# Performance work log

Hardware: AMD Instinct MI355X
Metric: run time of the kernel (lower is better)

## Reference

```python
import jax, jax.numpy as jnp
import numpy as np

B = 1024
IN_Q = 2048
IN_KV = 2048
NH = 16
D = 64
INNER = NH * D
TF = 4
NC = 2
EPS = 1e-5
SLOPE = 0.01  # LeakyReLU default negative slope


def setup_inputs() -> dict:
    key = jax.random.key(0)
    ks = jax.random.split(key, 8)
    s = 0.02
    return {
        "q_input": jax.random.normal(ks[0], (B, IN_Q), jnp.float32),
        "kv_input": jax.random.normal(ks[1], (B, IN_KV), jnp.float32),
        "Wq": jax.random.normal(ks[2], (INNER, IN_Q), jnp.float32) * s,
        "bq": jax.random.normal(ks[3], (INNER,), jnp.float32) * s,
        "Wkv": jax.random.normal(ks[4], (2 * INNER, IN_KV), jnp.float32) * s,
        "bkv": jax.random.normal(ks[5], (2 * INNER,), jnp.float32) * s,
        "bn_w": jnp.ones((TF,), jnp.float32),
        "bn_b": jnp.zeros((TF,), jnp.float32),
        "Wo": jax.random.normal(ks[6], (NC, TF), jnp.float32) * s,
        "bo": jax.random.normal(ks[7], (NC,), jnp.float32) * s,
    }


def reference(q_input, kv_input, Wq, bq, Wkv, bkv, bn_w, bn_b, Wo, bo):
    b = q_input.shape[0]
    # projections: [B, NH, D] and [B, NH, 2D]
    q = (q_input @ Wq.T + bq).reshape(b, NH, D)
    kv = (kv_input @ Wkv.T + bkv).reshape(b, NH, 2 * D)
    k, v = kv[..., :D], kv[..., D:]
    # sim[b,n] = k[b,n,:] . q[b,n,:]  (per-head scalar score)
    sim = jnp.einsum("bnd,bnd->bn", k, q)
    att = jax.nn.softmax(sim, axis=-1)  # softmax over heads
    # torch.matmul([B,NH], [B,NH,D]) broadcast -> out[i,j,:] = sum_n att[j,n] v[i,n,:]
    att_out = jnp.einsum("jn,ind->ijd", att, v)  # [B, B, D]
    flat = att_out.reshape(b, b * D)  # [B, B*D]
    # AdaptiveAvgPool1d to TF bins (L % TF == 0 -> exact reshape-mean)
    pooled = flat.reshape(b, TF, (b * D) // TF).mean(axis=-1)  # [B, TF]
    x = jnp.where(pooled >= 0, pooled, SLOPE * pooled)  # LeakyReLU
    # BatchNorm1d, train mode (batch stats, biased variance)
    mean = x.mean(axis=0)
    var = x.var(axis=0)
    x = (x - mean) * jax.lax.rsqrt(var + EPS) * bn_w + bn_b
    # dropout(p=0.0) is identity
    return x @ Wo.T + bo  # [B, NC]
```

## Files before the change

kernel.cpp:

```cpp
#include <hip/hip_runtime.h>
#include <hip/hip_bf16.h>

#define EPS 1e-5f
#define SLOPE 0.01f

typedef __attribute__((ext_vector_type(8))) short bfrag8;
typedef __attribute__((ext_vector_type(4))) float f32x4;

#define WS_SIM_OFF   0u
#define WS_S_OFF     65536u
#define WS_WVS_OFF   131072u
#define WS_BVS_OFF   262144u
#define WS_AIMG_OFF  262208u
#define WS_BIMG_OFF  8650816u

__device__ __forceinline__ unsigned short f2bf(float f) {
    union { float f; unsigned int u; } x; x.f = f;
    unsigned int r = (x.u + 0x7FFFu + ((x.u >> 16) & 1u)) >> 16;
    return (unsigned short)r;
}
__device__ __forceinline__ uint4 pack8(const float4& a, const float4& b) {
    uint4 r;
    r.x = (unsigned)f2bf(a.x) | ((unsigned)f2bf(a.y) << 16);
    r.y = (unsigned)f2bf(a.z) | ((unsigned)f2bf(a.w) << 16);
    r.z = (unsigned)f2bf(b.x) | ((unsigned)f2bf(b.y) << 16);
    r.w = (unsigned)f2bf(b.z) | ((unsigned)f2bf(b.w) << 16);
    return r;
}

#define PREP_A   524288
#define PREP_B2  (PREP_A + 524288)
#define PREP_WVSE (PREP_B2 + 32768)
#define PREP_SIME (PREP_WVSE + 16384)
#define PREP_END  (PREP_SIME + 16)

__global__ __launch_bounds__(256) void prep_kernel(
        const float* __restrict__ qin, const float* __restrict__ kvin,
        const float* __restrict__ Wq, const float* __restrict__ Wkv,
        const float* __restrict__ bkv, unsigned char* __restrict__ ws) {
    int gid = blockIdx.x * 256 + threadIdx.x;
    if (gid < PREP_A) {
        int l  = gid & 63;
        int mi = (gid >> 6) & 1;
        int ks = (gid >> 7) & 1;
        int kt = (gid >> 8) & 31;
        int rm = (gid >> 13) & 1;
        int mbb = (gid >> 14) & 15;
        int qq = gid >> 18;
        int row = mbb * 64 + rm * 32 + mi * 16 + (l & 15);
        int k0  = kt * 64 + ks * 32 + (l >> 4) * 8;
        const float* src = (qq ? kvin : qin) + (size_t)row * 2048 + k0;
        float4 v0 = *(const float4*)src;
        float4 v1 = *(const float4*)(src + 4);
        *(uint4*)(ws + WS_AIMG_OFF + (size_t)gid * 16) = pack8(v0, v1);
    } else if (gid < PREP_B2) {
        int g2 = gid - PREP_A;
        int l  = g2 & 63;
        int ni = (g2 >> 6) & 1;
        int ks = (g2 >> 7) & 1;
        int kt = (g2 >> 8) & 31;
        int dww = (g2 >> 13) & 1;
        int qq  = (g2 >> 14) & 1;
        int hh  = g2 >> 15;
        int col = qq * 64 + dww * 32 + ni * 16 + (l & 15);
        int k0  = kt * 64 + ks * 32 + (l >> 4) * 8;
        const float* wrow = (col < 64) ? (Wq  + (size_t)(hh * 64 + col) * 2048)
                                       : (Wkv + (size_t)(hh * 128 + (col - 64)) * 2048);
        float4 v0 = *(const float4*)(wrow + k0);
        float4 v1 = *(const float4*)(wrow + k0 + 4);
        *(uint4*)(ws + WS_BIMG_OFF + (size_t)g2 * 16) = pack8(v0, v1);
    } else if (gid < PREP_WVSE) {
        int g2 = gid - PREP_B2;
        int n = g2 >> 11, c = g2 & 2047;
        const float* base = Wkv + (size_t)(n * 128 + 64) * 2048 + c;
        float s = 0.f;
        #pragma unroll 8
        for (int d = 0; d < 64; ++d) s += base[(size_t)d * 2048];
        ((float*)(ws + WS_WVS_OFF))[c * 16 + n] = s;
    } else if (gid < PREP_SIME) {
        ((float*)(ws + WS_SIM_OFF))[gid - PREP_WVSE] = 0.f;
    } else if (gid < PREP_END) {
        int n = gid - PREP_SIME;
        float b = 0.f;
        #pragma unroll
        for (int d = 0; d < 64; ++d) b += bkv[n * 128 + 64 + d];
        ((float*)(ws + WS_BVS_OFF))[n] = b;
    }
}

__global__ __launch_bounds__(512) void gemm_sim_kernel(
        const float* __restrict__ bq, const float* __restrict__ bkv,
        unsigned char* __restrict__ ws) {
    __shared__ alignas(16) float Cqs[2][2][32][32];

    const int t = threadIdx.x;
    const int w = t >> 6, l = t & 63;
    const int h = blockIdx.x, mb = blockIdx.y;
    const int m0 = mb * 64;
    const int qk = w >> 2, rm = (w >> 1) & 1, dw = w & 1;
    const int lrow = l & 15;

    const unsigned char* aP = ws + WS_AIMG_OFF
        + (size_t)(((qk * 16 + mb) * 2 + rm) * 32) * 4096 + l * 16;
    const unsigned char* bP = ws + WS_BIMG_OFF
        + (size_t)(((h * 2 + qk) * 2 + dw) * 32) * 4096 + l * 16;
    float* sim = (float*)(ws + WS_SIM_OFF);

    f32x4 acc00 = (f32x4)0.f, acc01 = (f32x4)0.f, acc10 = (f32x4)0.f, acc11 = (f32x4)0.f;

#define DECL_SET(S) bfrag8 S##a00, S##a01, S##a10, S##a11, S##b00, S##b01, S##b10, S##b11
#define LOADS(kt, S) do {                                                     \
    const unsigned char* _a = aP + (size_t)(kt) * 4096;                       \
    const unsigned char* _b = bP + (size_t)(kt) * 4096;                       \
    S##a00 = *(const bfrag8*)(_a);                                            \
    S##a01 = *(const bfrag8*)(_a + 1024);                                     \
    S##a10 = *(const bfrag8*)(_a + 2048);                                     \
    S##a11 = *(const bfrag8*)(_a + 3072);                                     \
    S##b00 = *(const bfrag8*)(_b);                                            \
    S##b01 = *(const bfrag8*)(_b + 1024);                                     \
    S##b10 = *(const bfrag8*)(_b + 2048);                                     \
    S##b11 = *(const bfrag8*)(_b + 3072);                                     \
} while (0)
#define COMP(S) do {                                                                        \
    acc00 = __builtin_amdgcn_mfma_f32_16x16x32_bf16(S##a00, S##b00, acc00, 0, 0, 0);        \
    acc01 = __builtin_amdgcn_mfma_f32_16x16x32_bf16(S##a00, S##b01, acc01, 0, 0, 0);        \
    acc10 = __builtin_amdgcn_mfma_f32_16x16x32_bf16(S##a01, S##b00, acc10, 0, 0, 0);        \
    acc11 = __builtin_amdgcn_mfma_f32_16x16x32_bf16(S##a01, S##b01, acc11, 0, 0, 0);        \
    acc00 = __builtin_amdgcn_mfma_f32_16x16x32_bf16(S##a10, S##b10, acc00, 0, 0, 0);        \
    acc01 = __builtin_amdgcn_mfma_f32_16x16x32_bf16(S##a10, S##b11, acc01, 0, 0, 0);        \
    acc10 = __builtin_amdgcn_mfma_f32_16x16x32_bf16(S##a11, S##b10, acc10, 0, 0, 0);        \
    acc11 = __builtin_amdgcn_mfma_f32_16x16x32_bf16(S##a11, S##b11, acc11, 0, 0, 0);        \
} while (0)

    DECL_SET(P0_); DECL_SET(P1_); DECL_SET(P2_);
    LOADS(0, P0_);
    LOADS(1, P1_);
    for (int kt = 0; kt < 30; kt += 3) {
        LOADS(kt + 2, P2_);  COMP(P0_);
        LOADS(kt + 3, P0_);  COMP(P1_);
        LOADS(kt + 4, P1_);  COMP(P2_);
    }
    COMP(P0_);
    COMP(P1_);
#undef DECL_SET
#undef LOADS
#undef COMP

    float biasv[2];
    #pragma unroll
    for (int ni = 0; ni < 2; ++ni) {
        int d = dw * 32 + ni * 16 + lrow;
        biasv[ni] = qk ? bkv[h * 128 + d] : bq[h * 64 + d];
    }
    f32x4 acc[2][2] = {{acc00, acc01}, {acc10, acc11}};
    #pragma unroll
    for (int mi = 0; mi < 2; ++mi)
        #pragma unroll
        for (int ni = 0; ni < 2; ++ni)
            #pragma unroll
            for (int r = 0; r < 4; ++r)
                acc[mi][ni][r] += biasv[ni];

    if (!qk) {
        #pragma unroll
        for (int mi = 0; mi < 2; ++mi)
            #pragma unroll
            for (int ni = 0; ni < 2; ++ni)
                #pragma unroll
                for (int r = 0; r < 4; ++r)
                    Cqs[rm][dw][mi * 16 + (l >> 4) * 4 + r][ni * 16 + lrow] = acc[mi][ni][r];
    }
    __syncthreads();
    if (qk) {
        #pragma unroll
        for (int mi = 0; mi < 2; ++mi) {
            float p[4];
            #pragma unroll
            for (int r = 0; r < 4; ++r) {
                int r32 = mi * 16 + (l >> 4) * 4 + r;
                p[r] = Cqs[rm][dw][r32][lrow]      * acc[mi][0][r]
                     + Cqs[rm][dw][r32][16 + lrow] * acc[mi][1][r];
            }
            #pragma unroll
            for (int r = 0; r < 4; ++r) {
                float v = p[r];
                v += __shfl_xor(v, 1); v += __shfl_xor(v, 2);
                v += __shfl_xor(v, 4); v += __shfl_xor(v, 8);
                if ((l & 15) == 0) {
                    int row = m0 + rm * 32 + mi * 16 + (l >> 4) * 4 + r;
                    atomicAdd(&sim[row * 16 + h], v);
                }
            }
        }
    }
}

__global__ __launch_bounds__(256) void s_kernel(
        const float* __restrict__ kvin, unsigned char* __restrict__ ws) {
    int b = blockIdx.x, t = threadIdx.x;
    int w = t >> 6, l = t & 63;
    __shared__ float SW[4][16];
    int n = t & 15, g = t >> 4;
    const float* kvrow = kvin + (size_t)b * 2048;
    const float* wv = (const float*)(ws + WS_WVS_OFF);
    float p = 0.f;
    #pragma unroll 4
    for (int tt = 0; tt < 128; ++tt) {
        int c = g + (tt << 4);
        p = fmaf(kvrow[c], wv[c * 16 + n], p);
    }
    p += __shfl_xor(p, 16);
    p += __shfl_xor(p, 32);
    if (l < 16) SW[w][n] = p;
    __syncthreads();
    if (t < 16) {
        float sv = SW[0][t] + SW[1][t] + SW[2][t] + SW[3][t]
                 + ((const float*)(ws + WS_BVS_OFF))[t];
        ((float*)(ws + WS_S_OFF))[b * 16 + t] = sv;
    }
}

__global__ __launch_bounds__(1024) void final_kernel(
        const float* __restrict__ bn_w, const float* __restrict__ bn_b,
        const float* __restrict__ Wo, const float* __restrict__ bo,
        const unsigned char* __restrict__ ws, float* __restrict__ out) {
    int t = threadIdx.x;
    int w = t >> 6;
    int l = t & 63;
    __shared__ float Aw[16][16];
    __shared__ float Af[4][16];
    __shared__ float SWs[16][8];
    __shared__ float FS[8];
    __shared__ float sc[4], sh[4];

    float a16[16];
    {
        const float* srow = (const float*)(ws + WS_SIM_OFF) + (size_t)t * 16;
        float4 v0 = *(const float4*)(srow + 0);
        float4 v1 = *(const float4*)(srow + 4);
        float4 v2 = *(const float4*)(srow + 8);
        float4 v3 = *(const float4*)(srow + 12);
        a16[0]=v0.x; a16[1]=v0.y; a16[2]=v0.z; a16[3]=v0.w;
        a16[4]=v1.x; a16[5]=v1.y; a16[6]=v1.z; a16[7]=v1.w;
        a16[8]=v2.x; a16[9]=v2.y; a16[10]=v2.z; a16[11]=v2.w;
        a16[12]=v3.x; a16[13]=v3.y; a16[14]=v3.z; a16[15]=v3.w;
        float m = a16[0];
        #pragma unroll
        for (int n = 1; n < 16; ++n) m = fmaxf(m, a16[n]);
        float den = 0.f;
        #pragma unroll
        for (int n = 0; n < 16; ++n) { a16[n] = expf(a16[n] - m); den += a16[n]; }
        float inv = 1.f / den;
        #pragma unroll
        for (int n = 0; n < 16; ++n) a16[n] *= inv;
    }
    #pragma unroll
    for (int n = 0; n < 16; ++n) {
        float p = a16[n];
        p += __shfl_xor(p, 1);  p += __shfl_xor(p, 2);
        p += __shfl_xor(p, 4);  p += __shfl_xor(p, 8);
        p += __shfl_xor(p, 16); p += __shfl_xor(p, 32);
        a16[n] = p;
    }
    if (l == 0) {
        #pragma unroll
        for (int n = 0; n < 16; ++n) Aw[w][n] = a16[n];
    }
    __syncthreads();
    if (t < 64) {
        int f = t >> 4, n = t & 15;
        Af[f][n] = Aw[4*f][n] + Aw[4*f+1][n] + Aw[4*f+2][n] + Aw[4*f+3][n];
    }
    __syncthreads();

    float sv[16];
    {
        const float* srow = (const float*)(ws + WS_S_OFF) + (size_t)t * 16;
        float4 v0 = *(const float4*)(srow + 0);
        float4 v1 = *(const float4*)(srow + 4);
        float4 v2 = *(const float4*)(srow + 8);
        float4 v3 = *(const float4*)(srow + 12);
        sv[0]=v0.x; sv[1]=v0.y; sv[2]=v0.z; sv[3]=v0.w;
        sv[4]=v1.x; sv[5]=v1.y; sv[6]=v1.z; sv[7]=v1.w;
        sv[8]=v2.x; sv[9]=v2.y; sv[10]=v2.z; sv[11]=v2.w;
        sv[12]=v3.x; sv[13]=v3.y; sv[14]=v3.z; sv[15]=v3.w;
    }
    float x[4];
    #pragma unroll
    for (int f = 0; f < 4; ++f) {
        float p = 0.f;
        #pragma unroll
        for (int n = 0; n < 16; ++n) p = fmaf(Af[f][n], sv[n], p);
        p *= (1.f / 16384.f);
        x[f] = (p >= 0.f) ? p : SLOPE * p;
    }

    float st[8];
    #pragma unroll
    for (int f = 0; f < 4; ++f) { st[f] = x[f]; st[4 + f] = x[f] * x[f]; }
    #pragma unroll
    for (int j = 0; j < 8; ++j) {
        float p = st[j];
        p += __shfl_xor(p, 1);  p += __shfl_xor(p, 2);
        p += __shfl_xor(p, 4);  p += __shfl_xor(p, 8);
        p += __shfl_xor(p, 16); p += __shfl_xor(p, 32);
        st[j] = p;
    }
    if (l == 0) {
        #pragma unroll
        for (int j = 0; j < 8; ++j) SWs[w][j] = st[j];
    }
    __syncthreads();
    if (t < 8) {
        float p = 0.f;
        #pragma unroll
        for (int ww = 0; ww < 16; ++ww) p += SWs[ww][t];
        FS[t] = p;
    }
    __syncthreads();
    if (t < 4) {
        float mean = FS[t] * (1.f / 1024.f);
        float var  = FS[4 + t] * (1.f / 1024.f) - mean * mean;
        float s = bn_w[t] / sqrtf(var + EPS);
        sc[t] = s;
        sh[t] = bn_b[t] - mean * s;
    }
    __syncthreads();

    float o0 = bo[0], o1 = bo[1];
    #pragma unroll
    for (int f = 0; f < 4; ++f) {
        float xh = x[f] * sc[f] + sh[f];
        o0 = fmaf(xh, Wo[f], o0);
        o1 = fmaf(xh, Wo[4 + f], o1);
    }
    *(float2*)(out + (size_t)t * 2) = make_float2(o0, o1);
}

extern "C" void kernel_launch(void* const* d_in, const int* in_sizes, int n_in,
                              void* d_out, int out_size, void* d_ws, size_t ws_size,
                              hipStream_t stream) {
    const float* q_input  = (const float*)d_in[0];
    const float* kv_input = (const float*)d_in[1];
    const float* Wq   = (const float*)d_in[2];
    const float* bq   = (const float*)d_in[3];
    const float* Wkv  = (const float*)d_in[4];
    const float* bkv  = (const float*)d_in[5];
    const float* bn_w = (const float*)d_in[6];
    const float* bn_b = (const float*)d_in[7];
    const float* Wo   = (const float*)d_in[8];
    const float* bo   = (const float*)d_in[9];
    float* out = (float*)d_out;
    unsigned char* ws = (unsigned char*)d_ws;

    hipLaunchKernelGGL(prep_kernel, dim3((PREP_END + 255) / 256), dim3(256), 0, stream,
                       q_input, kv_input, Wq, Wkv, bkv, ws);
    hipLaunchKernelGGL(gemm_sim_kernel, dim3(16, 16), dim3(512), 0, stream,
                       bq, bkv, ws);
    hipLaunchKernelGGL(s_kernel, dim3(1024), dim3(256), 0, stream, kv_input, ws);
    hipLaunchKernelGGL(final_kernel, dim3(1), dim3(1024), 0, stream,
                       bn_w, bn_b, Wo, bo, ws, out);
}
```

Measured before the change: 66.59 us.

## Restructure Q/K projection into LDS-staged tiled GEMM with separate sim kernel

Replaces the fused per-head GEMM+sim kernel, which read bf16 fragments straight from global memory, with a standard tiled GEMM. Each 64x64 output tile is staged in LDS through double-buffered global_load_lds using an XOR-swizzled layout, and prep now packs the images in that order. The Q/K projections go to a workspace buffer, and a new per-row kernel adds the biases and reduces q·k per head, which removes the atomics and the sim zeroing. This costs an extra kernel launch and a 8 MB fp32 round trip through global memory.

```diff
diff --git a/kernel.cpp b/kernel.cpp
--- a/kernel.cpp
+++ b/kernel.cpp
@@ -6,13 +6,17 @@
 
 typedef __attribute__((ext_vector_type(8))) short bfrag8;
 typedef __attribute__((ext_vector_type(4))) float f32x4;
+
+#define AS1 __attribute__((address_space(1)))
+#define AS3 __attribute__((address_space(3)))
 
 #define WS_SIM_OFF   0u
 #define WS_S_OFF     65536u
 #define WS_WVS_OFF   131072u
 #define WS_BVS_OFF   262144u
-#define WS_AIMG_OFF  262208u
-#define WS_BIMG_OFF  8650816u
+#define WS_OUT_OFF   262208u
+#define WS_AIMG_OFF  8650816u
+#define WS_BIMG_OFF  25428032u
 
 __device__ __forceinline__ unsigned short f2bf(float f) {
     union { float f; unsigned int u; } x; x.f = f;
@@ -28,11 +32,10 @@
     return r;
 }
 
-#define PREP_A   524288
-#define PREP_B2  (PREP_A + 524288)
+#define PREP_A    524288
+#define PREP_B2   (PREP_A + 524288)
 #define PREP_WVSE (PREP_B2 + 32768)
-#define PREP_SIME (PREP_WVSE + 16384)
-#define PREP_END  (PREP_SIME + 16)
+#define PREP_END  (PREP_WVSE + 16)
 
 __global__ __launch_bounds__(256) void prep_kernel(
         const float* __restrict__ qin, const float* __restrict__ kvin,
@@ -40,34 +43,35 @@
         const float* __restrict__ bkv, unsigned char* __restrict__ ws) {
     int gid = blockIdx.x * 256 + threadIdx.x;
     if (gid < PREP_A) {
-        int l  = gid & 63;
-        int mi = (gid >> 6) & 1;
-        int ks = (gid >> 7) & 1;
-        int kt = (gid >> 8) & 31;
-        int rm = (gid >> 13) & 1;
-        int mbb = (gid >> 14) & 15;
-        int qq = gid >> 18;
-        int row = mbb * 64 + rm * 32 + mi * 16 + (l & 15);
-        int k0  = kt * 64 + ks * 32 + (l >> 4) * 8;
-        const float* src = (qq ? kvin : qin) + (size_t)row * 2048 + k0;
+        int p  = gid & 511;
+        int kt = (gid >> 9) & 31;
+        int mt = (gid >> 14) & 15;
+        int s2 = gid >> 18;
+        int rit = p >> 3;
+        int gk = (p & 7) ^ (rit & 7);
+        int row = mt * 64 + rit;
+        int k = kt * 64 + gk * 8;
+        const float* src = (s2 ? kvin : qin) + (size_t)row * 2048 + k;
         float4 v0 = *(const float4*)src;
         float4 v1 = *(const float4*)(src + 4);
         *(uint4*)(ws + WS_AIMG_OFF + (size_t)gid * 16) = pack8(v0, v1);
     } else if (gid < PREP_B2) {
         int g2 = gid - PREP_A;
-        int l  = g2 & 63;
-        int ni = (g2 >> 6) & 1;
-        int ks = (g2 >> 7) & 1;
-        int kt = (g2 >> 8) & 31;
-        int dww = (g2 >> 13) & 1;
-        int qq  = (g2 >> 14) & 1;
-        int hh  = g2 >> 15;
-        int col = qq * 64 + dww * 32 + ni * 16 + (l & 15);
-        int k0  = kt * 64 + ks * 32 + (l >> 4) * 8;
-        const float* wrow = (col < 64) ? (Wq  + (size_t)(hh * 64 + col) * 2048)
-                                       : (Wkv + (size_t)(hh * 128 + (col - 64)) * 2048);
-        float4 v0 = *(const float4*)(wrow + k0);
-        float4 v1 = *(const float4*)(wrow + k0 + 4);
+        int p  = g2 & 511;
+        int kt = (g2 >> 9) & 31;
+        int nt = g2 >> 14;
+        int cit = p >> 3;
+        int gk = (p & 7) ^ (cit & 7);
+        int col = nt * 64 + cit;
+        int k = kt * 64 + gk * 8;
+        const float* wrow;
+        if (col < 1024) wrow = Wq + (size_t)col * 2048;
+        else {
+            int c2 = col - 1024;
+            wrow = Wkv + (size_t)(((c2 >> 6) << 7) + (c2 & 63)) * 2048;
+        }
+        float4 v0 = *(const float4*)(wrow + k);
+        float4 v1 = *(const float4*)(wrow + k + 4);
         *(uint4*)(ws + WS_BIMG_OFF + (size_t)g2 * 16) = pack8(v0, v1);
     } else if (gid < PREP_WVSE) {
         int g2 = gid - PREP_B2;
@@ -77,10 +81,8 @@
         #pragma unroll 8
         for (int d = 0; d < 64; ++d) s += base[(size_t)d * 2048];
         ((float*)(ws + WS_WVS_OFF))[c * 16 + n] = s;
-    } else if (gid < PREP_SIME) {
-        ((float*)(ws + WS_SIM_OFF))[gid - PREP_WVSE] = 0.f;
     } else if (gid < PREP_END) {
-        int n = gid - PREP_SIME;
+        int n = gid - PREP_WVSE;
         float b = 0.f;
         #pragma unroll
         for (int d = 0; d < 64; ++d) b += bkv[n * 128 + 64 + d];
@@ -88,110 +90,109 @@
     }
 }
 
-__global__ __launch_bounds__(512) void gemm_sim_kernel(
+__global__ __launch_bounds__(256) void gemm_qk_kernel(unsigned char* __restrict__ ws) {
+    __shared__ alignas(16) unsigned short LA[2][4096];
+    __shared__ alignas(16) unsigned short LB[2][4096];
+
+    const int t = threadIdx.x;
+    const int w = t >> 6, l = t & 63;
+    const int nt = blockIdx.x, mt = blockIdx.y;
+    const int wr = w >> 1, wc = w & 1;
+    const int lrow = l & 15, lhi = l >> 4;
+
+    const unsigned char* aBase = ws + WS_AIMG_OFF
+        + (size_t)((nt >= 16) ? 4194304u : 0u) + (size_t)mt * 262144u;
+    const unsigned char* bBase = ws + WS_BIMG_OFF + (size_t)nt * 262144u;
+    float* Out = (float*)(ws + WS_OUT_OFF);
+
+    int offA[2][2], offB[2][2];
+    #pragma unroll
+    for (int ks = 0; ks < 2; ++ks)
+        #pragma unroll
+        for (int i = 0; i < 2; ++i) {
+            int rA = wr * 32 + i * 16 + lrow;
+            int rB = wc * 32 + i * 16 + lrow;
+            offA[ks][i] = rA * 128 + (((ks * 4 + lhi) ^ (rA & 7)) << 4);
+            offB[ks][i] = rB * 128 + (((ks * 4 + lhi) ^ (rB & 7)) << 4);
+        }
+
+    f32x4 acc00 = (f32x4)0.f, acc01 = (f32x4)0.f, acc10 = (f32x4)0.f, acc11 = (f32x4)0.f;
+
+#define STAGE(kt_, buf_) do {                                                        \
+    const unsigned char* _as = aBase + (size_t)(kt_) * 8192;                         \
+    const unsigned char* _bs = bBase + (size_t)(kt_) * 8192;                         \
+    unsigned char* _ad = ((unsigned char*)&LA[0][0]) + (buf_) * 8192;                \
+    unsigned char* _bd = ((unsigned char*)&LB[0][0]) + (buf_) * 8192;                \
+    _Pragma("unroll")                                                                \
+    for (int _j = 0; _j < 2; ++_j) {                                                 \
+        int _p = _j * 256 + t;                                                       \
+        __builtin_amdgcn_global_load_lds(                                            \
+            (const AS1 unsigned int*)(const void*)(_as + _p * 16),                   \
+            (AS3 unsigned int*)(void*)(_ad + _p * 16), 16, 0, 0);                    \
+        __builtin_amdgcn_global_load_lds(                                            \
+            (const AS1 unsigned int*)(const void*)(_bs + _p * 16),                   \
+            (AS3 unsigned int*)(void*)(_bd + _p * 16), 16, 0, 0);                    \
+    } } while (0)
+
+    STAGE(0, 0);
+    __syncthreads();
+
+    for (int kt = 0; kt < 32; ++kt) {
+        const int cur = kt & 1;
+        if (kt < 31) STAGE(kt + 1, cur ^ 1);
+        const char* la = (const char*)&LA[0][0] + cur * 8192;
+        const char* lb = (const char*)&LB[0][0] + cur * 8192;
+        bfrag8 fa00 = *(const bfrag8*)(la + offA[0][0]);
+        bfrag8 fa01 = *(const bfrag8*)(la + offA[0][1]);
+        bfrag8 fa10 = *(const bfrag8*)(la + offA[1][0]);
+        bfrag8 fa11 = *(const bfrag8*)(la + offA[1][1]);
+        bfrag8 fb00 = *(const bfrag8*)(lb + offB[0][0]);
+        bfrag8 fb01 = *(const bfrag8*)(lb + offB[0][1]);
+        bfrag8 fb10 = *(const bfrag8*)(lb + offB[1][0]);
+        bfrag8 fb11 = *(const bfrag8*)(lb + offB[1][1]);
+        acc00 = __builtin_amdgcn_mfma_f32_16x16x32_bf16(fa00, fb00, acc00, 0, 0, 0);
+        acc01 = __builtin_amdgcn_mfma_f32_16x16x32_bf16(fa00, fb01, acc01, 0, 0, 0);
+        acc10 = __builtin_amdgcn_mfma_f32_16x16x32_bf16(fa01, fb00, acc10, 0, 0, 0);
+        acc11 = __builtin_amdgcn_mfma_f32_16x16x32_bf16(fa01, fb01, acc11, 0, 0, 0);
+        acc00 = __builtin_amdgcn_mfma_f32_16x16x32_bf16(fa10, fb10, acc00, 0, 0, 0);
+        acc01 = __builtin_amdgcn_mfma_f32_16x16x32_bf16(fa10, fb11, acc01, 0, 0, 0);
+        acc10 = __builtin_amdgcn_mfma_f32_16x16x32_bf16(fa11, fb10, acc10, 0, 0, 0);
+        acc11 = __builtin_amdgcn_mfma_f32_16x16x32_bf16(fa11, fb11, acc11, 0, 0, 0);
+        __syncthreads();
+    }
+#undef STAGE
+
+    f32x4 acc[2][2] = {{acc00, acc01}, {acc10, acc11}};
+    #pragma unroll
+    for (int mi = 0; mi < 2; ++mi)
+        #pragma unroll
+        for (int ni = 0; ni < 2; ++ni) {
+            int col = nt * 64 + wc * 32 + ni * 16 + lrow;
+            #pragma unroll
+            for (int r = 0; r < 4; ++r) {
+                int row = mt * 64 + wr * 32 + mi * 16 + lhi * 4 + r;
+                Out[(size_t)row * 2048 + col] = acc[mi][ni][r];
+            }
+        }
+}
+
+__global__ __launch_bounds__(256) void sim_kernel(
         const float* __restrict__ bq, const float* __restrict__ bkv,
         unsigned char* __restrict__ ws) {
-    __shared__ alignas(16) float Cqs[2][2][32][32];
-
-    const int t = threadIdx.x;
-    const int w = t >> 6, l = t & 63;
-    const int h = blockIdx.x, mb = blockIdx.y;
-    const int m0 = mb * 64;
-    const int qk = w >> 2, rm = (w >> 1) & 1, dw = w & 1;
-    const int lrow = l & 15;
-
-    const unsigned char* aP = ws + WS_AIMG_OFF
-        + (size_t)(((qk * 16 + mb) * 2 + rm) * 32) * 4096 + l * 16;
-    const unsigned char* bP = ws + WS_BIMG_OFF
-        + (size_t)(((h * 2 + qk) * 2 + dw) * 32) * 4096 + l * 16;
+    int b = blockIdx.x, t = threadIdx.x;
+    int w = t >> 6, d = t & 63;
+    const float* orow = (const float*)(ws + WS_OUT_OFF) + (size_t)b * 2048;
     float* sim = (float*)(ws + WS_SIM_OFF);
-
-    f32x4 acc00 = (f32x4)0.f, acc01 = (f32x4)0.f, acc10 = (f32x4)0.f, acc11 = (f32x4)0.f;
-
-#define DECL_SET(S) bfrag8 S##a00, S##a01, S##a10, S##a11, S##b00, S##b01, S##b10, S##b11
-#define LOADS(kt, S) do {                                                     \
-    const unsigned char* _a = aP + (size_t)(kt) * 4096;                       \
-    const unsigned char* _b = bP + (size_t)(kt) * 4096;                       \
-    S##a00 = *(const bfrag8*)(_a);                                            \
-    S##a01 = *(const bfrag8*)(_a + 1024);                                     \
-    S##a10 = *(const bfrag8*)(_a + 2048);                                     \
-    S##a11 = *(const bfrag8*)(_a + 3072);                                     \
-    S##b00 = *(const bfrag8*)(_b);                                            \
-    S##b01 = *(const bfrag8*)(_b + 1024);                                     \
-    S##b10 = *(const bfrag8*)(_b + 2048);                                     \
-    S##b11 = *(const bfrag8*)(_b + 3072);                                     \
-} while (0)
-#define COMP(S) do {                                                                        \
-    acc00 = __builtin_amdgcn_mfma_f32_16x16x32_bf16(S##a00, S##b00, acc00, 0, 0, 0);        \
-    acc01 = __builtin_amdgcn_mfma_f32_16x16x32_bf16(S##a00, S##b01, acc01, 0, 0, 0);        \
-    acc10 = __builtin_amdgcn_mfma_f32_16x16x32_bf16(S##a01, S##b00, acc10, 0, 0, 0);        \
-    acc11 = __builtin_amdgcn_mfma_f32_16x16x32_bf16(S##a01, S##b01, acc11, 0, 0, 0);        \
-    acc00 = __builtin_amdgcn_mfma_f32_16x16x32_bf16(S##a10, S##b10, acc00, 0, 0, 0);        \
-    acc01 = __builtin_amdgcn_mfma_f32_16x16x32_bf16(S##a10, S##b11, acc01, 0, 0, 0);        \
-    acc10 = __builtin_amdgcn_mfma_f32_16x16x32_bf16(S##a11, S##b10, acc10, 0, 0, 0);        \
-    acc11 = __builtin_amdgcn_mfma_f32_16x16x32_bf16(S##a11, S##b11, acc11, 0, 0, 0);        \
-} while (0)
-
-    DECL_SET(P0_); DECL_SET(P1_); DECL_SET(P2_);
-    LOADS(0, P0_);
-    LOADS(1, P1_);
-    for (int kt = 0; kt < 30; kt += 3) {
-        LOADS(kt + 2, P2_);  COMP(P0_);
-        LOADS(kt + 3, P0_);  COMP(P1_);
-        LOADS(kt + 4, P1_);  COMP(P2_);
-    }
-    COMP(P0_);
-    COMP(P1_);
-#undef DECL_SET
-#undef LOADS
-#undef COMP
-
-    float biasv[2];
-    #pragma unroll
-    for (int ni = 0; ni < 2; ++ni) {
-        int d = dw * 32 + ni * 16 + lrow;
-        biasv[ni] = qk ? bkv[h * 128 + d] : bq[h * 64 + d];
-    }
-    f32x4 acc[2][2] = {{acc00, acc01}, {acc10, acc11}};
-    #pragma unroll
-    for (int mi = 0; mi < 2; ++mi)
-        #pragma unroll
-        for (int ni = 0; ni < 2; ++ni)
-            #pragma unroll
-            for (int r = 0; r < 4; ++r)
-                acc[mi][ni][r] += biasv[ni];
-
-    if (!qk) {
-        #pragma unroll
-        for (int mi = 0; mi < 2; ++mi)
-            #pragma unroll
-            for (int ni = 0; ni < 2; ++ni)
-                #pragma unroll
-                for (int r = 0; r < 4; ++r)
-                    Cqs[rm][dw][mi * 16 + (l >> 4) * 4 + r][ni * 16 + lrow] = acc[mi][ni][r];
-    }
-    __syncthreads();
-    if (qk) {
-        #pragma unroll
-        for (int mi = 0; mi < 2; ++mi) {
-            float p[4];
-            #pragma unroll
-            for (int r = 0; r < 4; ++r) {
-                int r32 = mi * 16 + (l >> 4) * 4 + r;
-                p[r] = Cqs[rm][dw][r32][lrow]      * acc[mi][0][r]
-                     + Cqs[rm][dw][r32][16 + lrow] * acc[mi][1][r];
-            }
-            #pragma unroll
-            for (int r = 0; r < 4; ++r) {
-                float v = p[r];
-                v += __shfl_xor(v, 1); v += __shfl_xor(v, 2);
-                v += __shfl_xor(v, 4); v += __shfl_xor(v, 8);
-                if ((l & 15) == 0) {
-                    int row = m0 + rm * 32 + mi * 16 + (l >> 4) * 4 + r;
-                    atomicAdd(&sim[row * 16 + h], v);
-                }
-            }
-        }
+    #pragma unroll
+    for (int hh = 0; hh < 4; ++hh) {
+        int h = w * 4 + hh;
+        float qv = orow[h * 64 + d]        + bq[h * 64 + d];
+        float kv = orow[1024 + h * 64 + d] + bkv[h * 128 + d];
+        float p = qv * kv;
+        p += __shfl_xor(p, 1);  p += __shfl_xor(p, 2);
+        p += __shfl_xor(p, 4);  p += __shfl_xor(p, 8);
+        p += __shfl_xor(p, 16); p += __shfl_xor(p, 32);
+        if (d == 0) sim[b * 16 + h] = p;
     }
 }
 
@@ -355,8 +356,8 @@
 
     hipLaunchKernelGGL(prep_kernel, dim3((PREP_END + 255) / 256), dim3(256), 0, stream,
                        q_input, kv_input, Wq, Wkv, bkv, ws);
-    hipLaunchKernelGGL(gemm_sim_kernel, dim3(16, 16), dim3(512), 0, stream,
-                       bq, bkv, ws);
+    hipLaunchKernelGGL(gemm_qk_kernel, dim3(32, 16), dim3(256), 0, stream, ws);
+    hipLaunchKernelGGL(sim_kernel, dim3(1024), dim3(256), 0, stream, bq, bkv, ws);
     hipLaunchKernelGGL(s_kernel, dim3(1024), dim3(256), 0, stream, kv_input, ws);
     hipLaunchKernelGGL(final_kernel, dim3(1), dim3(1024), 0, stream,
                        bn_w, bn_b, Wo, bo, ws, out);
```

Result: slower. 72.43 us (+8.8%).
